# Kernel tuning notes

Hardware: AMD Instinct MI355X
Metric: run time of the kernel (lower is better)

Reference implementation:

```python
import jax, jax.numpy as jnp
import numpy as np
from jax import lax

KERNEL_SIZE = 3  # matches init_kwargs


def setup_inputs() -> dict:
    key = jax.random.key(0)
    heatmap = jax.random.normal(key, (8, 16, 512, 512), dtype=jnp.float32)
    return {"heatmap": heatmap, "max_peaks": 262144}


def reference(heatmap, max_peaks):
    """Peak detection: local maxima of 3x3 neighborhood that are > 0.

    Returns:
      peaks:  (B, max_peaks, 3) float32, rows [x, y, confidence] packed in
              (channel, row-major) order (identical ordering to the torch
              per-channel torch.where + cat), zero-padded after counts[b].
      counts: (B,) int32, number of valid peak rows per batch item.
    """
    k = KERNEL_SIZE
    pad = (k - 1) // 2
    # max_pool2d(stride=1, padding=pad) pads with -inf implicitly
    max_pooled = lax.reduce_window(
        heatmap, -jnp.inf, lax.max,
        window_dimensions=(1, 1, k, k),
        window_strides=(1, 1, 1, 1),
        padding=[(0, 0), (0, 0), (pad, pad), (pad, pad)],
    )
    peak_mask = (heatmap == max_pooled) & (heatmap > 0)

    B, C, H, W = heatmap.shape
    n = C * H * W
    flat_mask = peak_mask.reshape(B, n)
    flat_val = heatmap.reshape(B, n)

    # Stream compaction: stable argsort moves valid flat indices (in order)
    # to the front; invalid entries get sentinel key n.
    idx = jnp.arange(n, dtype=jnp.int32)
    keys = jnp.where(flat_mask, idx, jnp.int32(n))
    order = jnp.argsort(keys, axis=1)[:, :max_peaks]  # (B, max_peaks)

    valid = jnp.take_along_axis(flat_mask, order, axis=1)
    conf = jnp.take_along_axis(flat_val, order, axis=1)
    x = (order % W).astype(heatmap.dtype)
    y = ((order // W) % H).astype(heatmap.dtype)

    peaks = jnp.where(valid[..., None], jnp.stack([x, y, conf], axis=-1), 0.0)
    counts = flat_mask.sum(axis=1).astype(jnp.int32)
    return peaks, counts
```

## Files before the change

### kernel.cpp

```cpp
#include <hip/hip_runtime.h>


namespace {
constexpr int kB = 8;
constexpr int kC = 16;
constexpr int kH = 512;
constexpr int kW = 512;
constexpr int kNPB = kC * kH * kW;
constexpr int kMaxPeaks = 262144;
constexpr int kRows = 8;
constexpr int kStripsPerBatch = kC * (kH / kRows);
constexpr int kNStrips = kB * kStripsPerBatch;
constexpr int kWPB = 4;
constexpr int kTPB = 64 * kWPB;
constexpr long long kPeaksElems = (long long)kB * kMaxPeaks * 3;
constexpr float kNeg = -3.402823466e38f;
}

__device__ __forceinline__ float fmax3(float a, float b, float c) {
  return fmaxf(fmaxf(a, b), c);
}

__device__ __forceinline__ void loadrow(const float* __restrict__ rp, int y0,
                                        int i, float d[8]) {
  const int yy = y0 + i;
  if (yy >= 0 && yy < kH) {
    const float4 q0 = *reinterpret_cast<const float4*>(rp + i * kW);
    const float4 q1 = *reinterpret_cast<const float4*>(rp + i * kW + 4);
    d[0] = q0.x; d[1] = q0.y; d[2] = q0.z; d[3] = q0.w;
    d[4] = q1.x; d[5] = q1.y; d[6] = q1.z; d[7] = q1.w;
  } else {
#pragma unroll
    for (int j = 0; j < 8; ++j) d[j] = kNeg;
  }
}

__global__ void __launch_bounds__(kTPB)
peak_count_kernel(const float* __restrict__ hm,
                  unsigned long long* __restrict__ bmw,
                  int* __restrict__ cnts) {
  const int t = threadIdx.x, lane = t & 63, wv = t >> 6;
  const int s = blockIdx.x * kWPB + wv;
  const int b = s >> 10;
  const int si = s & 1023;
  const int c = si >> 6;
  const int y0 = (si & 63) * kRows;
  const float* rp = hm + (long long)b * kNPB + c * (kH * kW) + y0 * kW + lane * 8;

  float A[8], Bv[8], Cv[8], N1[8], N2[8];
  loadrow(rp, y0, -1, A);
  loadrow(rp, y0, 0, Bv);
  loadrow(rp, y0, 1, Cv);
  loadrow(rp, y0, 2, N1);
  loadrow(rp, y0, 3, N2);

  unsigned long long myword = 0;
  int scnt = 0;
#pragma unroll
  for (int r = 0; r < kRows; ++r) {
    float cm[8];
#pragma unroll
    for (int j = 0; j < 8; ++j) cm[j] = fmax3(A[j], Bv[j], Cv[j]);
    float hl = __shfl_up(cm[7], 1, 64);
    float hr = __shfl_down(cm[0], 1, 64);
    if (lane == 0) hl = kNeg;
    if (lane == 63) hr = kNeg;
    float m[8];
    m[0] = fmax3(hl, cm[0], cm[1]);
#pragma unroll
    for (int j = 1; j < 7; ++j) m[j] = fmax3(cm[j - 1], cm[j], cm[j + 1]);
    m[7] = fmax3(cm[6], cm[7], hr);
#pragma unroll
    for (int j = 0; j < 8; ++j) {
      const float v = Bv[j];
      const unsigned long long wj = __ballot((v == m[j]) && (v > 0.0f));
      scnt += (int)__popcll(wj);
      if (lane == r * 8 + j) myword = wj;
    }
#pragma unroll
    for (int j = 0; j < 8; ++j) { A[j] = Bv[j]; Bv[j] = Cv[j]; Cv[j] = N1[j]; N1[j] = N2[j]; }
    if (r <= 4) loadrow(rp, y0, r + 4, N2);
  }
  bmw[(long long)s * 64 + lane] = myword;
  if (lane == 0) cnts[s] = scnt;
}

__global__ void __launch_bounds__(kTPB)
peak_write_kernel(const float* __restrict__ hm,
                  const unsigned long long* __restrict__ bmw,
                  const int* __restrict__ cnts,
                  float* __restrict__ out) {
  __shared__ int s_pre[kWPB], s_tot[kWPB], s_c[kWPB];
  __shared__ unsigned long long s_w[kWPB][64];
  const int t = threadIdx.x, lane = t & 63, wv = t >> 6;
  const int g = blockIdx.x;
  const int b = g >> 8;
  const int g0 = (g & 255) * kWPB;
  const int* cb = cnts + b * kStripsPerBatch;

  const int4 c4 = *reinterpret_cast<const int4*>(cb + t * 4);
  const int idx0 = t * 4;
  int tot = c4.x + c4.y + c4.z + c4.w;
  int pre = (idx0 < g0) ? tot : 0;
  if (idx0 == g0) { s_c[0] = c4.x; s_c[1] = c4.y; s_c[2] = c4.z; s_c[3] = c4.w; }
#pragma unroll
  for (int d = 32; d >= 1; d >>= 1) {
    pre += __shfl_down(pre, d, 64);
    tot += __shfl_down(tot, d, 64);
  }
  if (lane == 0) { s_pre[wv] = pre; s_tot[wv] = tot; }
  __syncthreads();
  const int base = s_pre[0] + s_pre[1] + s_pre[2] + s_pre[3];
  if (g0 == 0 && t == 0)
    out[kPeaksElems + b] =
        (float)(s_tot[0] + s_tot[1] + s_tot[2] + s_tot[3]);

  int off0 = base;
  for (int k = 0; k < wv; ++k) off0 += s_c[k];
  if (off0 >= kMaxPeaks) return;

  const int s = b * kStripsPerBatch + g0 + wv;
  const int si = g0 + wv, c = si >> 6, y0 = (si & 63) * kRows;
  const float* rp = hm + (long long)b * kNPB + c * (kH * kW) + y0 * kW + lane * 8;

  s_w[wv][lane] = bmw[(long long)s * 64 + lane];

  float P0[8], P1[8], cur[8];
  loadrow(rp, y0, 0, P0);
  loadrow(rp, y0, 1, P1);

  const unsigned long long pm = (lane == 0) ? 0ull : (~0ull >> (64 - lane));
  int rbase = off0;
  float* pb = out + (long long)b * kMaxPeaks * 3;
#pragma unroll
  for (int r = 0; r < kRows; ++r) {
#pragma unroll
    for (int j = 0; j < 8; ++j) { cur[j] = P0[j]; P0[j] = P1[j]; }
    if (r < kRows - 2) loadrow(rp, y0, r + 2, P1);

    unsigned long long w[8];
#pragma unroll
    for (int j = 0; j < 8; ++j) w[j] = s_w[wv][r * 8 + j];
    int lexcl = 0, rowcnt = 0;
#pragma unroll
    for (int j = 0; j < 8; ++j) {
      lexcl += (int)__popcll(w[j] & pm);
      rowcnt += (int)__popcll(w[j]);
    }
    int rank = rbase + lexcl;
    const float fy = (float)(y0 + r);
#pragma unroll
    for (int j = 0; j < 8; ++j) {
      const int f = (int)((w[j] >> lane) & 1);
      if (f && rank < kMaxPeaks) {
        float* o = pb + (long long)rank * 3;
        o[0] = (float)(lane * 8 + j);
        o[1] = fy;
        o[2] = cur[j];
      }
      rank += f;
    }
    rbase += rowcnt;
    if (rbase >= kMaxPeaks) break;
  }
}

extern "C" void kernel_launch(void* const* d_in, const int* in_sizes, int n_in,
                              void* d_out, int out_size, void* d_ws, size_t ws_size,
                              hipStream_t stream) {
  const float* hm = (const float*)d_in[0];
  float* out = (float*)d_out;

  unsigned long long* bmw = (unsigned long long*)d_ws;
  int* cnts = (int*)(bmw + (long long)kNStrips * 64);

  peak_count_kernel<<<kNStrips / kWPB, kTPB, 0, stream>>>(hm, bmw, cnts);
  peak_write_kernel<<<kNStrips / kWPB, kTPB, 0, stream>>>(hm, bmw, cnts, out);
}
```

Baseline: 219.7 us.

## Record packed peaks per strip in first pass, scatter them in second

The first pass now computes each peak's local rank within its strip and writes packed 64-bit records (confidence, y, x) to a per-strip workspace buffer. The second pass only prefix-sums the strip counts and copies records contiguously to the output, so it no longer re-reads the heatmap or decodes bitmasks. This avoids a second full read of the heatmap. In exchange it needs a large workspace and adds scattered record writes. It falls back to the old path when the workspace is too small.

```diff
diff --git a/kernel.cpp b/kernel.cpp
--- a/kernel.cpp
+++ b/kernel.cpp
@@ -13,6 +13,7 @@
 constexpr int kNStrips = kB * kStripsPerBatch;
 constexpr int kWPB = 4;
 constexpr int kTPB = 64 * kWPB;
+constexpr int kCap = kRows * kW;
 constexpr long long kPeaksElems = (long long)kB * kMaxPeaks * 3;
 constexpr float kNeg = -3.402823466e38f;
 }
@@ -34,6 +35,119 @@
     for (int j = 0; j < 8; ++j) d[j] = kNeg;
   }
 }
+
+
+__global__ void __launch_bounds__(kTPB)
+peak_record_kernel(const float* __restrict__ hm,
+                   unsigned long long* __restrict__ rec,
+                   int* __restrict__ cnts) {
+  const int t = threadIdx.x, lane = t & 63, wv = t >> 6;
+  const int s = blockIdx.x * kWPB + wv;
+  const int b = s >> 10;
+  const int si = s & 1023;
+  const int c = si >> 6;
+  const int y0 = (si & 63) * kRows;
+  const float* rp = hm + (long long)b * kNPB + c * (kH * kW) + y0 * kW + lane * 8;
+  unsigned long long* rb = rec + (long long)s * kCap;
+
+  float A[8], Bv[8], Cv[8], N1[8], N2[8];
+  loadrow(rp, y0, -1, A);
+  loadrow(rp, y0, 0, Bv);
+  loadrow(rp, y0, 1, Cv);
+  loadrow(rp, y0, 2, N1);
+  loadrow(rp, y0, 3, N2);
+
+  const unsigned long long pm = (lane == 0) ? 0ull : (~0ull >> (64 - lane));
+  int rbase = 0;
+#pragma unroll
+  for (int r = 0; r < kRows; ++r) {
+    float cm[8];
+#pragma unroll
+    for (int j = 0; j < 8; ++j) cm[j] = fmax3(A[j], Bv[j], Cv[j]);
+    float hl = __shfl_up(cm[7], 1, 64);
+    float hr = __shfl_down(cm[0], 1, 64);
+    if (lane == 0) hl = kNeg;
+    if (lane == 63) hr = kNeg;
+    float m[8];
+    m[0] = fmax3(hl, cm[0], cm[1]);
+#pragma unroll
+    for (int j = 1; j < 7; ++j) m[j] = fmax3(cm[j - 1], cm[j], cm[j + 1]);
+    m[7] = fmax3(cm[6], cm[7], hr);
+
+    unsigned long long w[8];
+    int lexcl = 0, rowcnt = 0;
+#pragma unroll
+    for (int j = 0; j < 8; ++j) {
+      const float v = Bv[j];
+      w[j] = __ballot((v == m[j]) && (v > 0.0f));
+      lexcl += (int)__popcll(w[j] & pm);
+      rowcnt += (int)__popcll(w[j]);
+    }
+    int rank = rbase + lexcl;
+    const unsigned yx = (unsigned)((y0 + r) << 16);
+#pragma unroll
+    for (int j = 0; j < 8; ++j) {
+      const int f = (int)((w[j] >> lane) & 1);
+      if (f) {
+        rb[rank] = ((unsigned long long)__float_as_uint(Bv[j]) << 32) |
+                   (unsigned long long)(yx | (unsigned)(lane * 8 + j));
+      }
+      rank += f;
+    }
+    rbase += rowcnt;
+
+#pragma unroll
+    for (int j = 0; j < 8; ++j) { A[j] = Bv[j]; Bv[j] = Cv[j]; Cv[j] = N1[j]; N1[j] = N2[j]; }
+    if (r <= 4) loadrow(rp, y0, r + 4, N2);
+  }
+  if (lane == 0) cnts[s] = rbase;
+}
+
+__global__ void __launch_bounds__(kTPB)
+peak_scatter_kernel(const unsigned long long* __restrict__ rec,
+                    const int* __restrict__ cnts,
+                    float* __restrict__ out) {
+  __shared__ int s_pre[kWPB], s_tot[kWPB], s_c[kWPB];
+  const int t = threadIdx.x, lane = t & 63, wv = t >> 6;
+  const int g = blockIdx.x;
+  const int b = g >> 8;
+  const int g0 = (g & 255) * kWPB;
+  const int* cb = cnts + b * kStripsPerBatch;
+
+  const int4 c4 = *reinterpret_cast<const int4*>(cb + t * 4);
+  const int idx0 = t * 4;
+  int tot = c4.x + c4.y + c4.z + c4.w;
+  int pre = (idx0 < g0) ? tot : 0;
+  if (idx0 == g0) { s_c[0] = c4.x; s_c[1] = c4.y; s_c[2] = c4.z; s_c[3] = c4.w; }
+#pragma unroll
+  for (int d = 32; d >= 1; d >>= 1) {
+    pre += __shfl_down(pre, d, 64);
+    tot += __shfl_down(tot, d, 64);
+  }
+  if (lane == 0) { s_pre[wv] = pre; s_tot[wv] = tot; }
+  __syncthreads();
+  const int base = s_pre[0] + s_pre[1] + s_pre[2] + s_pre[3];
+  if (g0 == 0 && t == 0)
+    out[kPeaksElems + b] =
+        (float)(s_tot[0] + s_tot[1] + s_tot[2] + s_tot[3]);
+
+  int off0 = base;
+  for (int k = 0; k < wv; ++k) off0 += s_c[k];
+  if (off0 >= kMaxPeaks) return;
+
+  const int s = b * kStripsPerBatch + g0 + wv;
+  const int lim = min(s_c[wv], kMaxPeaks - off0);
+  const unsigned long long* rb = rec + (long long)s * kCap;
+  float* o = out + (long long)b * kMaxPeaks * 3 + (long long)off0 * 3;
+  for (int i = lane; i < lim; i += 64) {
+    const unsigned long long v = rb[i];
+    float* p = o + (long long)i * 3;
+    p[0] = (float)(unsigned)(v & 0xffffu);
+    p[1] = (float)(unsigned)((v >> 16) & 0xffffu);
+    p[2] = __uint_as_float((unsigned)(v >> 32));
+  }
+}
+
 
 __global__ void __launch_bounds__(kTPB)
 peak_count_kernel(const float* __restrict__ hm,
@@ -171,9 +285,19 @@
   const float* hm = (const float*)d_in[0];
   float* out = (float*)d_out;
 
-  unsigned long long* bmw = (unsigned long long*)d_ws;
-  int* cnts = (int*)(bmw + (long long)kNStrips * 64);
-
-  peak_count_kernel<<<kNStrips / kWPB, kTPB, 0, stream>>>(hm, bmw, cnts);
-  peak_write_kernel<<<kNStrips / kWPB, kTPB, 0, stream>>>(hm, bmw, cnts, out);
-}
+  const size_t rec_bytes =
+      (size_t)kNStrips * (size_t)kCap * sizeof(unsigned long long);
+  const size_t need = rec_bytes + (size_t)kNStrips * sizeof(int);
+
+  if (ws_size >= need) {
+    unsigned long long* rec = (unsigned long long*)d_ws;
+    int* cnts = (int*)((char*)d_ws + rec_bytes);
+    peak_record_kernel<<<kNStrips / kWPB, kTPB, 0, stream>>>(hm, rec, cnts);
+    peak_scatter_kernel<<<kNStrips / kWPB, kTPB, 0, stream>>>(rec, cnts, out);
+  } else {
+    unsigned long long* bmw = (unsigned long long*)d_ws;
+    int* cnts = (int*)(bmw + (long long)kNStrips * 64);
+    peak_count_kernel<<<kNStrips / kWPB, kTPB, 0, stream>>>(hm, bmw, cnts);
+    peak_write_kernel<<<kNStrips / kWPB, kTPB, 0, stream>>>(hm, bmw, cnts, out);
+  }
+}
```

After: 219.3 us. About the same (-0.2%).
